# Performance work log

Hardware: AMD Instinct MI355X
Metric: run time of the kernel (lower is better)

Reference implementation:

```python
import jax, jax.numpy as jnp
import numpy as np

B, S, HID = 2, 2048, 2048
H, K, D = 32, 8, 64          # query heads, kv heads, head_dim
G = H // K                   # GQA group size
ROPE_MSCALE = 1.2            # constant rope_mscale applied to q and k
SM_SCALE = 1.0 / (D ** 0.5)  # flash_attn default softmax scale


def rotate_half(x):
    h = x.shape[-1] // 2
    return jnp.concatenate([-x[..., h:], x[..., :h]], axis=-1)


def setup_inputs() -> dict:
    key = jax.random.key(0)
    k1, k2, k3, k4 = jax.random.split(key, 4)
    hidden_states = jax.random.normal(k1, (B, S, HID), dtype=jnp.float32)
    # standard rotary tables: cos/sin of shape [S, D]
    inv_freq = 1.0 / (10000.0 ** (jnp.arange(0, D, 2, dtype=jnp.float32) / D))
    freqs = jnp.outer(jnp.arange(S, dtype=jnp.float32), inv_freq)  # [S, D/2]
    emb = jnp.concatenate([freqs, freqs], axis=-1)                 # [S, D]
    cos, sin = jnp.cos(emb), jnp.sin(emb)
    per_head_scale = 1.0 + 0.1 * jax.random.normal(k2, (B, H), dtype=jnp.float32)
    Wqkv = jax.random.normal(k3, ((H + 2 * K) * D, HID), dtype=jnp.float32) * (HID ** -0.5)
    Wo = jax.random.normal(k4, (HID, H * D), dtype=jnp.float32) * ((H * D) ** -0.5)
    return {"cos": cos, "sin": sin, "hidden_states": hidden_states,
            "per_head_scale": per_head_scale, "Wqkv": Wqkv, "Wo": Wo}


def reference(cos, sin, hidden_states, per_head_scale, Wqkv, Wo):
    # fused QKV projection (CastedLinear, no bias)
    qkv = jnp.einsum('bsh,oh->bso', hidden_states, Wqkv)          # [B,S,(H+2K)*D]
    qkv = qkv.reshape(B, S, H + 2 * K, D)
    q = qkv[:, :, :H]                 # [B,S,H,D]
    k = qkv[:, :, H:H + K]            # [B,S,K,D]
    v = qkv[:, :, H + K:]             # [B,S,K,D]
    # rotary embedding: cos/sin [S,D] -> broadcast over heads via [S,1,D]
    c = cos[:, None, :]
    s_ = sin[:, None, :]
    q = q * c + rotate_half(q) * s_
    k = k * c + rotate_half(k) * s_
    # rope_mscale
    q = q * ROPE_MSCALE
    k = k * ROPE_MSCALE
    # per-head scale on queries: [B,H] -> [B,1,H,1]
    q = q * per_head_scale[:, None, :, None]
    # GQA attention without materializing repeated K/V: group query heads
    qg = q.reshape(B, S, K, G, D)
    scores = jnp.einsum('bqkgd,bskd->bkgqs', qg, k) * SM_SCALE    # [B,K,G,Sq,Sk]
    causal = jnp.arange(S)[:, None] >= jnp.arange(S)[None, :]     # [Sq,Sk]
    scores = jnp.where(causal, scores, jnp.finfo(scores.dtype).min)
    probs = jax.nn.softmax(scores, axis=-1)
    out = jnp.einsum('bkgqs,bskd->bqkgd', probs, v).reshape(B, S, H * D)
    return jnp.einsum('bso,ho->bsh', out, Wo)                     # o_proj
```

## Files before the change

### kernel.cpp

```cpp
#include <hip/hip_runtime.h>
#include <stdint.h>

typedef unsigned short u16;
typedef short short8 __attribute__((ext_vector_type(8)));
typedef float f32x4 __attribute__((ext_vector_type(4)));
typedef uint32_t u32x4 __attribute__((ext_vector_type(4)));

#define S_LEN 2048
#define NQH 32
#define NKH 8
#define DHD 64
#define MNEG -1.0e30f

__device__ __forceinline__ float b2f(u16 u){
  union { uint32_t i; float f; } c; c.i = ((uint32_t)u) << 16; return c.f;
}
__device__ __forceinline__ u16 f2b(float f){
  union { float f; uint32_t i; } c; c.f = f;
  uint32_t r = c.i + 0x7fffu + ((c.i >> 16) & 1u);
  return (u16)(r >> 16);
}
__device__ __forceinline__ uint32_t cvt_pk_bf16(float lo, float hi){
  uint32_t r;
  asm("v_cvt_pk_bf16_f32 %0, %1, %2" : "=v"(r) : "v"(lo), "v"(hi));
  return r;
}
__device__ __forceinline__ void gload_lds16(const void* g, void* l){
  __builtin_amdgcn_global_load_lds((const __attribute__((address_space(1))) uint32_t*)g,
                                   (__attribute__((address_space(3))) uint32_t*)l, 16, 0, 0);
}

__global__ __launch_bounds__(256) void cvt_all(const float* __restrict__ hs,
                                               const float* __restrict__ wq,
                                               const float* __restrict__ wo,
                                               const float* __restrict__ cosp,
                                               const float* __restrict__ sinp,
                                               u16* __restrict__ hsB,
                                               u16* __restrict__ wqB,
                                               u16* __restrict__ woB,
                                               uint32_t* __restrict__ csB){
  int i = blockIdx.x * 256 + threadIdx.x;
  if (i >= 4718592){
    int off = i - 4718592;
    float4 c = ((const float4*)cosp)[off];
    float4 s = ((const float4*)sinp)[off];
    u32x4 o = { (uint32_t)f2b(c.x) | ((uint32_t)f2b(s.x) << 16),
                (uint32_t)f2b(c.y) | ((uint32_t)f2b(s.y) << 16),
                (uint32_t)f2b(c.z) | ((uint32_t)f2b(s.z) << 16),
                (uint32_t)f2b(c.w) | ((uint32_t)f2b(s.w) << 16) };
    ((u32x4*)csB)[off] = o;
    return;
  }
  const float* src; u16* dst; int off;
  if (i < 2097152)      { src = hs; dst = hsB; off = i; }
  else if (i < 3670016) { src = wq; dst = wqB; off = i - 2097152; }
  else                  { src = wo; dst = woB; off = i - 3670016; }
  float4 v = ((const float4*)src)[off];
  uint2 o;
  o.x = (uint32_t)f2b(v.x) | ((uint32_t)f2b(v.y) << 16);
  o.y = (uint32_t)f2b(v.z) | ((uint32_t)f2b(v.w) << 16);
  ((uint2*)dst)[off] = o;
}

template<int OUT_F32>
__global__ __launch_bounds__(256)
void gemm_bt(const u16* __restrict__ A, const u16* __restrict__ Bm,
             void* __restrict__ Cp, int N, int K)
{
  __shared__ alignas(16) u16 lA[128 * 64];
  __shared__ alignas(16) u16 lB[128 * 64];
  const int tid = threadIdx.x;
  const int w = tid >> 6, l = tid & 63;
  const int lg = l >> 4, lc = l & 15;
  const int wm = w >> 1, wn = w & 1;
  const int m0 = blockIdx.y * 128, n0 = blockIdx.x * 128;
  const int srow = l >> 3, sc = l & 7;
  const size_t ldb = (size_t)K * 2;
  f32x4 acc[4][4] = {};
  const int kiters = K >> 6;
  for (int kt = 0; kt < kiters; ++kt){
    __syncthreads();
#pragma unroll
    for (int i = 0; i < 4; ++i){
      const int row = (i * 4 + w) * 8 + srow;
      const int gc = ((sc ^ (row & 7)) << 4);
      gload_lds16((const char*)A + (size_t)(m0 + row) * ldb + (size_t)kt * 128 + gc,
                  (char*)lA + row * 128 + sc * 16);
    }
#pragma unroll
    for (int i = 0; i < 4; ++i){
      const int row = (i * 4 + w) * 8 + srow;
      const int gc = ((sc ^ (row & 7)) << 4);
      gload_lds16((const char*)Bm + (size_t)(n0 + row) * ldb + (size_t)kt * 128 + gc,
                  (char*)lB + row * 128 + sc * 16);
    }
    __syncthreads();
#pragma unroll
    for (int kk = 0; kk < 2; ++kk){
      short8 af[4], bfr[4];
#pragma unroll
      for (int mi = 0; mi < 4; ++mi){
        const int row = wm * 64 + mi * 16 + lc;
        const int cc = (kk * 4 + lg) ^ (row & 7);
        af[mi] = *(const short8*)((const char*)lA + row * 128 + cc * 16);
      }
#pragma unroll
      for (int ni = 0; ni < 4; ++ni){
        const int row = wn * 64 + ni * 16 + lc;
        const int cc = (kk * 4 + lg) ^ (row & 7);
        bfr[ni] = *(const short8*)((const char*)lB + row * 128 + cc * 16);
      }
#pragma unroll
      for (int mi = 0; mi < 4; ++mi)
#pragma unroll
        for (int ni = 0; ni < 4; ++ni)
          acc[mi][ni] = __builtin_amdgcn_mfma_f32_16x16x32_bf16(af[mi], bfr[ni], acc[mi][ni], 0, 0, 0);
    }
  }
  const int r0 = m0 + wm * 64 + lg * 4;
  const int c0 = n0 + wn * 64 + lc;
#pragma unroll
  for (int mi = 0; mi < 4; ++mi)
#pragma unroll
    for (int ni = 0; ni < 4; ++ni)
#pragma unroll
      for (int j = 0; j < 4; ++j){
        const size_t idx = (size_t)(r0 + mi * 16 + j) * (size_t)N + (size_t)(c0 + ni * 16);
        if (OUT_F32) ((float*)Cp)[idx] = acc[mi][ni][j];
        else         ((u16*)Cp)[idx]  = f2b(acc[mi][ni][j]);
      }
}

__global__ __launch_bounds__(256)
void gemm1_rope(const u16* __restrict__ A, const u16* __restrict__ Bm,
                const uint32_t* __restrict__ cs, const float* __restrict__ phs,
                u16* __restrict__ Qo, u16* __restrict__ Ko, u16* __restrict__ Vraw)
{
  __shared__ alignas(16) u16 lA[128 * 64];
  __shared__ alignas(16) u16 lB[128 * 64];
  const int tid = threadIdx.x;
  const int w = tid >> 6, l = tid & 63;
  const int lg = l >> 4, lc = l & 15;
  const int wm = w >> 1, wn = w & 1;
  const int m0 = blockIdx.y * 128, n0 = blockIdx.x * 128;
  const int srow = l >> 3, sc = l & 7;
  const size_t ldb = 4096;
  f32x4 acc[4][4] = {};
  for (int kt = 0; kt < 32; ++kt){
    __syncthreads();
#pragma unroll
    for (int i = 0; i < 4; ++i){
      const int row = (i * 4 + w) * 8 + srow;
      const int gc = ((sc ^ (row & 7)) << 4);
      gload_lds16((const char*)A + (size_t)(m0 + row) * ldb + (size_t)kt * 128 + gc,
                  (char*)lA + row * 128 + sc * 16);
    }
#pragma unroll
    for (int i = 0; i < 4; ++i){
      const int row = (i * 4 + w) * 8 + srow;
      const int gc = ((sc ^ (row & 7)) << 4);
      gload_lds16((const char*)Bm + (size_t)(n0 + row) * ldb + (size_t)kt * 128 + gc,
                  (char*)lB + row * 128 + sc * 16);
    }
    __syncthreads();
#pragma unroll
    for (int kk = 0; kk < 2; ++kk){
      short8 af[4], bfr[4];
#pragma unroll
      for (int mi = 0; mi < 4; ++mi){
        const int row = wm * 64 + mi * 16 + lc;
        const int cc = (kk * 4 + lg) ^ (row & 7);
        af[mi] = *(const short8*)((const char*)lA + row * 128 + cc * 16);
      }
#pragma unroll
      for (int ni = 0; ni < 4; ++ni){
        const int row = wn * 64 + ni * 16 + lc;
        const int cc = (kk * 4 + lg) ^ (row & 7);
        bfr[ni] = *(const short8*)((const char*)lB + row * 128 + cc * 16);
      }
#pragma unroll
      for (int mi = 0; mi < 4; ++mi)
#pragma unroll
        for (int ni = 0; ni < 4; ++ni)
          acc[mi][ni] = __builtin_amdgcn_mfma_f32_16x16x32_bf16(af[mi], bfr[ni], acc[mi][ni], 0, 0, 0);
    }
  }
  const int r0 = m0 + wm * 64 + lg * 4;
  const int c0 = n0 + wn * 64 + lc;
  const int head = (n0 + wn * 64) >> 6;
  const int b = m0 >> 11;
  if (head < 40){
    const float scale = (head < NQH) ? 1.2f * 0.18033688011112042f * phs[b * NQH + head] : 1.2f;
    u16* dstbase = (head < NQH)
        ? (Qo + ((size_t)(b * NQH + head) * S_LEN) * 64)
        : (Ko + ((size_t)(b * NKH + (head - NQH)) * S_LEN) * 64);
#pragma unroll
    for (int mi = 0; mi < 4; ++mi)
#pragma unroll
      for (int j = 0; j < 4; ++j){
        const int s = (r0 + mi * 16 + j) & 2047;
        const uint32_t* csrow = cs + s * 64;
        float xs[4] = {acc[mi][0][j], acc[mi][1][j], acc[mi][2][j], acc[mi][3][j]};
#pragma unroll
        for (int ni = 0; ni < 4; ++ni){
          const int d = lc + ni * 16;
          const uint32_t csv = csrow[d];
          const float cv = b2f((u16)(csv & 0xffff));
          const float sv = b2f((u16)(csv >> 16));
          const float sgn = (ni < 2) ? -1.f : 1.f;
          const float v = (xs[ni] * cv + sgn * xs[ni ^ 2] * sv) * scale;
          dstbase[(size_t)s * 64 + d] = f2b(v);
        }
      }
  } else {
#pragma unroll
    for (int mi = 0; mi < 4; ++mi)
#pragma unroll
      for (int ni = 0; ni < 4; ++ni)
#pragma unroll
        for (int j = 0; j < 4; ++j){
          const int r = r0 + mi * 16 + j;
          Vraw[(size_t)r * 512 + (c0 + ni * 16 - 2560)] = f2b(acc[mi][ni][j]);
        }
  }
}

__global__ __launch_bounds__(256)
void vtrans(const u16* __restrict__ Vraw, u16* __restrict__ VT)
{
  int bid = blockIdx.x;
  int t = bid & 15, kh = (bid >> 4) & 7, b = bid >> 7;
  __shared__ u16 vlds[128][72];
  int tid = threadIdx.x;
  {
    int r = tid >> 1, half = tid & 1;
    const u16* src = Vraw + (((size_t)(b * S_LEN + t * 128 + r) * 8 + kh) << 6) + half * 32;
    uint4 a0 = *(const uint4*)(src);
    uint4 a1 = *(const uint4*)(src + 8);
    uint4 a2 = *(const uint4*)(src + 16);
    uint4 a3 = *(const uint4*)(src + 24);
    *(uint4*)&vlds[r][half * 32]      = a0;
    *(uint4*)&vlds[r][half * 32 + 8]  = a1;
    *(uint4*)&vlds[r][half * 32 + 16] = a2;
    *(uint4*)&vlds[r][half * 32 + 24] = a3;
  }
  __syncthreads();
  const int d = tid >> 2, kk2 = tid & 3;
  u16* dst = VT + ((size_t)(b * NKH + kh) * 64 + d) * S_LEN + t * 128 + kk2 * 32;
#pragma unroll
  for (int j = 0; j < 4; ++j){
    u16 o[8];
#pragma unroll
    for (int e = 0; e < 8; ++e){
      const int hk = kk2 * 32 + ((e >> 2) << 4) + j * 4 + (e & 3);
      o[e] = vlds[hk][d];
    }
    uint4 ov = { (uint32_t)o[0] | ((uint32_t)o[1] << 16), (uint32_t)o[2] | ((uint32_t)o[3] << 16),
                 (uint32_t)o[4] | ((uint32_t)o[5] << 16), (uint32_t)o[6] | ((uint32_t)o[7] << 16) };
    *(uint4*)(dst + j * 8) = ov;
  }
}

__device__ __forceinline__ void proc_chunk(f32x4 (&sv)[8], float& mrow, float& lsum,
                                           f32x4 (&o)[4], uint32_t (&pw)[4][4],
                                           const int lg, const int lc,
                                           const bool diag, const int qloc)
{
  if (diag){
#pragma unroll
    for (int nj = 0; nj < 8; ++nj)
#pragma unroll
      for (int jj = 0; jj < 4; ++jj){
        const int kloc = nj * 16 + lg * 4 + jj;
        if (kloc > qloc) sv[nj][jj] = MNEG;
      }
  }
  float mu = sv[0][0];
#pragma unroll
  for (int nj = 0; nj < 8; ++nj)
#pragma unroll
    for (int jj = 0; jj < 4; ++jj) mu = fmaxf(mu, sv[nj][jj]);
  mu = fmaxf(mu, __shfl_xor(mu, 16));
  mu = fmaxf(mu, __shfl_xor(mu, 32));
  if (!__all(mu <= mrow + 11.54f)){
    const float mnew = fmaxf(mrow, mu);
    const float sf = __builtin_amdgcn_exp2f(mrow - mnew);
    mrow = mnew;
    lsum *= sf;
#pragma unroll
    for (int dn = 0; dn < 4; ++dn)
#pragma unroll
      for (int jj = 0; jj < 4; ++jj) o[dn][jj] *= sf;
  }
  const float mcur = mrow;
  float ps = 0.f;
#pragma unroll
  for (int nj = 0; nj < 8; ++nj)
#pragma unroll
    for (int jj = 0; jj < 4; ++jj){
      const float pv = __builtin_amdgcn_exp2f(sv[nj][jj] - mcur);
      sv[nj][jj] = pv;
      ps += pv;
    }
  lsum += ps;
#pragma unroll
  for (int kk2 = 0; kk2 < 4; ++kk2){
    pw[kk2][0] = cvt_pk_bf16(sv[kk2 * 2][0],     sv[kk2 * 2][1]);
    pw[kk2][1] = cvt_pk_bf16(sv[kk2 * 2][2],     sv[kk2 * 2][3]);
    pw[kk2][2] = cvt_pk_bf16(sv[kk2 * 2 + 1][0], sv[kk2 * 2 + 1][1]);
    pw[kk2][3] = cvt_pk_bf16(sv[kk2 * 2 + 1][2], sv[kk2 * 2 + 1][3]);
  }
}

__device__ __forceinline__ short8 pw_frag(const uint32_t* pw){
  u32x4 v = { pw[0], pw[1], pw[2], pw[3] };
  return __builtin_bit_cast(short8, v);
}

__global__ __launch_bounds__(512, 2)
void attn_kernel(const u16* __restrict__ Q, const u16* __restrict__ Kr,
                 const u16* __restrict__ VT, u16* __restrict__ Ao)
{
  int bid = blockIdx.x;
  int p  = bid & 15;
  int gp = (bid >> 4) & 1;
  int kh = (bid >> 5) & 7;
  int b  = bid >> 8;
  const int qt0 = p, qt1 = 31 - p;

  __shared__ alignas(16) u16 lK[2][128 * 64];
  __shared__ alignas(16) u16 lV[2][64 * 128];

  const int tid = threadIdx.x;
  const int hh = tid >> 8;
  const int h  = kh * 4 + gp * 2 + hh;
  const int w  = (tid >> 6) & 3;
  const int l  = tid & 63;
  const int lg = l >> 4, lc = l & 15;

  short8 qf[2][2];
  {
    const u16* qbase = Q + ((size_t)(b * NQH + h) * S_LEN) * 64;
#pragma unroll
    for (int kk = 0; kk < 2; ++kk){
      qf[0][kk] = *(const short8*)(qbase + (size_t)(qt0 * 64 + w * 16 + lc) * 64 + kk * 32 + lg * 8);
      qf[1][kk] = *(const short8*)(qbase + (size_t)(qt1 * 64 + w * 16 + lc) * 64 + kk * 32 + lg * 8);
    }
  }

  const u16* Kb = Kr + (size_t)(b * NKH + kh) * S_LEN * 64;
  const u16* Vb = VT + (size_t)(b * NKH + kh) * 64 * S_LEN;

  f32x4 o[2][4] = {};
  float mrow[2] = {MNEG, MNEG};
  float lsum[2] = {0.f, 0.f};

  const int nt = (qt1 >> 1) + 1;
  const int nt0 = qt0 >> 1;

#define STAGE(T, BSEL) do { \
    _Pragma("unroll") \
    for (int i_ = 0; i_ < 2; ++i_){ \
      const int row_ = i_ * 64 + (tid >> 3); \
      const int ch_  = tid & 7; \
      const int gc_  = ((ch_ ^ (row_ & 7)) << 4); \
      gload_lds16((const char*)(Kb + (size_t)((T) * 128 + row_) * 64) + gc_, \
                  (char*)lK[BSEL] + row_ * 128 + ch_ * 16); \
    } \
    _Pragma("unroll") \
    for (int i_ = 0; i_ < 2; ++i_){ \
      const int row_ = i_ * 32 + (tid >> 4); \
      const int ch_  = tid & 15; \
      const int gc_  = ((ch_ ^ (row_ & 15)) << 4); \
      gload_lds16((const char*)(Vb + (size_t)row_ * S_LEN + (T) * 128) + gc_, \
                  (char*)lV[BSEL] + row_ * 256 + ch_ * 16); \
    } \
  } while (0)

  STAGE(0, 0);

  for (int t = 0; t < nt; ++t){
    const int cur = t & 1;
    const bool act0 = (t <= nt0);
    if (t + 1 < nt){
      STAGE(t + 1, cur ^ 1);
      asm volatile("s_waitcnt vmcnt(4)" ::: "memory");
    } else {
      asm volatile("s_waitcnt vmcnt(0)" ::: "memory");
    }
    __builtin_amdgcn_s_barrier();

    f32x4 sv[2][8] = {};
    __builtin_amdgcn_s_setprio(1);
#pragma unroll
    for (int kk = 0; kk < 2; ++kk){
      short8 kf[8];
#pragma unroll
      for (int nj = 0; nj < 8; ++nj){
        const int row = nj * 16 + lc;
        const int cc = (kk * 4 + lg) ^ (row & 7);
        kf[nj] = *(const short8*)((const char*)lK[cur] + row * 128 + cc * 16);
      }
      if (act0)
#pragma unroll
        for (int nj = 0; nj < 8; ++nj)
          sv[0][nj] = __builtin_amdgcn_mfma_f32_16x16x32_bf16(kf[nj], qf[0][kk], sv[0][nj], 0, 0, 0);
#pragma unroll
      for (int nj = 0; nj < 8; ++nj)
        sv[1][nj] = __builtin_amdgcn_mfma_f32_16x16x32_bf16(kf[nj], qf[1][kk], sv[1][nj], 0, 0, 0);
    }
    __builtin_amdgcn_s_setprio(0);

    uint32_t pw[2][4][4];
    if (act0)
      proc_chunk(sv[0], mrow[0], lsum[0], o[0], pw[0], lg, lc,
                 t == (qt0 >> 1), (qt0 & 1) * 64 + w * 16 + lc);
    proc_chunk(sv[1], mrow[1], lsum[1], o[1], pw[1], lg, lc,
               t == (qt1 >> 1), (qt1 & 1) * 64 + w * 16 + lc);

    __builtin_amdgcn_s_setprio(1);
#pragma unroll
    for (int kk2 = 0; kk2 < 4; ++kk2){
      short8 vf[4];
#pragma unroll
      for (int dn = 0; dn < 4; ++dn){
        const int row = dn * 16 + lc;
        const int cc = (kk2 * 4 + lg) ^ (row & 15);
        vf[dn] = *(const short8*)((const char*)lV[cur] + row * 256 + cc * 16);
      }
      if (act0){
        const short8 pb0 = pw_frag(pw[0][kk2]);
#pragma unroll
        for (int dn = 0; dn < 4; ++dn)
          o[0][dn] = __builtin_amdgcn_mfma_f32_16x16x32_bf16(vf[dn], pb0, o[0][dn], 0, 0, 0);
      }
      const short8 pb1 = pw_frag(pw[1][kk2]);
#pragma unroll
      for (int dn = 0; dn < 4; ++dn)
        o[1][dn] = __builtin_amdgcn_mfma_f32_16x16x32_bf16(vf[dn], pb1, o[1][dn], 0, 0, 0);
    }
    __builtin_amdgcn_s_setprio(0);
    __builtin_amdgcn_s_barrier();
  }
#undef STAGE

#pragma unroll
  for (int c = 0; c < 2; ++c){
    const int qt = c ? qt1 : qt0;
    float ls = lsum[c];
    ls += __shfl_xor(ls, 16);
    ls += __shfl_xor(ls, 32);
    const float inv = 1.f / ls;
    const int sq = qt * 64 + w * 16 + lc;
#pragma unroll
    for (int dn = 0; dn < 4; ++dn){
      uint2 pk;
      pk.x = cvt_pk_bf16(o[c][dn][0] * inv, o[c][dn][1] * inv);
      pk.y = cvt_pk_bf16(o[c][dn][2] * inv, o[c][dn][3] * inv);
      const int col = h * 64 + dn * 16 + lg * 4;
      *(uint2*)&Ao[(size_t)(b * S_LEN + sq) * 2048 + col] = pk;
    }
  }
}

extern "C" void kernel_launch(void* const* d_in, const int* in_sizes, int n_in,
                              void* d_out, int out_size, void* d_ws, size_t ws_size,
                              hipStream_t stream)
{
  const float* cosT = (const float*)d_in[0];
  const float* sinT = (const float*)d_in[1];
  const float* hs   = (const float*)d_in[2];
  const float* phs  = (const float*)d_in[3];
  const float* Wqkv = (const float*)d_in[4];
  const float* Wo   = (const float*)d_in[5];
  float* out = (float*)d_out;
  char* ws = (char*)d_ws;

  u16* hsB   = (u16*)(ws);
  u16* WqkvB = (u16*)(ws + 16777216);
  u16* WoB   = (u16*)(ws + 29360128);
  u16* Vraw  = (u16*)(ws + 37748736);
  u16* Qb    = (u16*)(ws + 41943040);
  u16* Kb    = (u16*)(ws + 58720256);
  u16* VTb   = (u16*)(ws + 62914560);
  uint32_t* csB = (uint32_t*)(ws + 67108864);
  u16* Ao    = hsB;

  cvt_all<<<18560, 256, 0, stream>>>(hs, Wqkv, Wo, cosT, sinT, hsB, WqkvB, WoB, csB);
  gemm1_rope<<<dim3(24, 32), 256, 0, stream>>>(hsB, WqkvB, csB, phs, Qb, Kb, Vraw);
  vtrans<<<256, 256, 0, stream>>>(Vraw, VTb);
  attn_kernel<<<512, 512, 0, stream>>>(Qb, Kb, VTb, Ao);
  gemm_bt<1><<<dim3(16, 32), 256, 0, stream>>>(Ao, WoB, (void*)out, 2048, 2048);
}
```

Before: 224.8 us.

## Double-buffer LDS in projection GEMMs and remap blocks for XCD locality

Both the QKV+RoPE GEMM and the output-projection GEMM now use two LDS buffers. The next K-tile's global-to-LDS loads are issued before the current tile's MFMAs, with a partial vmcnt wait, so memory latency overlaps compute. Launches also change to a 1D grid with a swizzled block-to-tile mapping that places neighbouring tiles on the same XCD to improve L2 reuse. LDS per block doubles to 64KB, which may reduce occupancy.

```diff
diff --git a/kernel.cpp b/kernel.cpp
--- a/kernel.cpp
+++ b/kernel.cpp
@@ -62,39 +62,51 @@
   ((uint2*)dst)[off] = o;
 }
 
-template<int OUT_F32>
+#define GSTAGE(KT, BSEL) do { \
+    _Pragma("unroll") \
+    for (int i_ = 0; i_ < 4; ++i_){ \
+      const int row_ = (i_ * 4 + w) * 8 + srow; \
+      const int gc_ = ((sc ^ (row_ & 7)) << 4); \
+      gload_lds16((const char*)A + (size_t)(m0 + row_) * ldb + (size_t)(KT) * 128 + gc_, \
+                  (char*)lA + (BSEL) * 16384 + row_ * 128 + sc * 16); \
+    } \
+    _Pragma("unroll") \
+    for (int i_ = 0; i_ < 4; ++i_){ \
+      const int row_ = (i_ * 4 + w) * 8 + srow; \
+      const int gc_ = ((sc ^ (row_ & 7)) << 4); \
+      gload_lds16((const char*)Bm + (size_t)(n0 + row_) * ldb + (size_t)(KT) * 128 + gc_, \
+                  (char*)lB + (BSEL) * 16384 + row_ * 128 + sc * 16); \
+    } \
+  } while (0)
+
 __global__ __launch_bounds__(256)
-void gemm_bt(const u16* __restrict__ A, const u16* __restrict__ Bm,
-             void* __restrict__ Cp, int N, int K)
+void gemm_bt_f32(const u16* __restrict__ A, const u16* __restrict__ Bm,
+                 float* __restrict__ Cp, int N, int K, int nbx, int nwg)
 {
-  __shared__ alignas(16) u16 lA[128 * 64];
-  __shared__ alignas(16) u16 lB[128 * 64];
+  __shared__ alignas(16) u16 lA[2 * 128 * 64];
+  __shared__ alignas(16) u16 lB[2 * 128 * 64];
+  const int id = blockIdx.x;
+  const int swz = (id & 7) * (nwg >> 3) + (id >> 3);
+  const int m0 = (swz / nbx) * 128, n0 = (swz % nbx) * 128;
   const int tid = threadIdx.x;
   const int w = tid >> 6, l = tid & 63;
   const int lg = l >> 4, lc = l & 15;
   const int wm = w >> 1, wn = w & 1;
-  const int m0 = blockIdx.y * 128, n0 = blockIdx.x * 128;
   const int srow = l >> 3, sc = l & 7;
   const size_t ldb = (size_t)K * 2;
   f32x4 acc[4][4] = {};
   const int kiters = K >> 6;
+
+  GSTAGE(0, 0);
   for (int kt = 0; kt < kiters; ++kt){
-    __syncthreads();
-#pragma unroll
-    for (int i = 0; i < 4; ++i){
-      const int row = (i * 4 + w) * 8 + srow;
-      const int gc = ((sc ^ (row & 7)) << 4);
-      gload_lds16((const char*)A + (size_t)(m0 + row) * ldb + (size_t)kt * 128 + gc,
-                  (char*)lA + row * 128 + sc * 16);
-    }
-#pragma unroll
-    for (int i = 0; i < 4; ++i){
-      const int row = (i * 4 + w) * 8 + srow;
-      const int gc = ((sc ^ (row & 7)) << 4);
-      gload_lds16((const char*)Bm + (size_t)(n0 + row) * ldb + (size_t)kt * 128 + gc,
-                  (char*)lB + row * 128 + sc * 16);
-    }
-    __syncthreads();
+    const int cur = kt & 1;
+    if (kt + 1 < kiters){
+      GSTAGE(kt + 1, cur ^ 1);
+      asm volatile("s_waitcnt vmcnt(8)" ::: "memory");
+    } else {
+      asm volatile("s_waitcnt vmcnt(0)" ::: "memory");
+    }
+    __builtin_amdgcn_s_barrier();
 #pragma unroll
     for (int kk = 0; kk < 2; ++kk){
       short8 af[4], bfr[4];
@@ -102,13 +114,13 @@
       for (int mi = 0; mi < 4; ++mi){
         const int row = wm * 64 + mi * 16 + lc;
         const int cc = (kk * 4 + lg) ^ (row & 7);
-        af[mi] = *(const short8*)((const char*)lA + row * 128 + cc * 16);
+        af[mi] = *(const short8*)((const char*)lA + cur * 16384 + row * 128 + cc * 16);
       }
 #pragma unroll
       for (int ni = 0; ni < 4; ++ni){
         const int row = wn * 64 + ni * 16 + lc;
         const int cc = (kk * 4 + lg) ^ (row & 7);
-        bfr[ni] = *(const short8*)((const char*)lB + row * 128 + cc * 16);
+        bfr[ni] = *(const short8*)((const char*)lB + cur * 16384 + row * 128 + cc * 16);
       }
 #pragma unroll
       for (int mi = 0; mi < 4; ++mi)
@@ -116,6 +128,7 @@
         for (int ni = 0; ni < 4; ++ni)
           acc[mi][ni] = __builtin_amdgcn_mfma_f32_16x16x32_bf16(af[mi], bfr[ni], acc[mi][ni], 0, 0, 0);
     }
+    __builtin_amdgcn_s_barrier();
   }
   const int r0 = m0 + wm * 64 + lg * 4;
   const int c0 = n0 + wn * 64 + lc;
@@ -124,11 +137,8 @@
 #pragma unroll
     for (int ni = 0; ni < 4; ++ni)
 #pragma unroll
-      for (int j = 0; j < 4; ++j){
-        const size_t idx = (size_t)(r0 + mi * 16 + j) * (size_t)N + (size_t)(c0 + ni * 16);
-        if (OUT_F32) ((float*)Cp)[idx] = acc[mi][ni][j];
-        else         ((u16*)Cp)[idx]  = f2b(acc[mi][ni][j]);
-      }
+      for (int j = 0; j < 4; ++j)
+        Cp[(size_t)(r0 + mi * 16 + j) * (size_t)N + (size_t)(c0 + ni * 16)] = acc[mi][ni][j];
 }
 
 __global__ __launch_bounds__(256)
@@ -136,33 +146,29 @@
                 const uint32_t* __restrict__ cs, const float* __restrict__ phs,
                 u16* __restrict__ Qo, u16* __restrict__ Ko, u16* __restrict__ Vraw)
 {
-  __shared__ alignas(16) u16 lA[128 * 64];
-  __shared__ alignas(16) u16 lB[128 * 64];
+  __shared__ alignas(16) u16 lA[2 * 128 * 64];
+  __shared__ alignas(16) u16 lB[2 * 128 * 64];
+  const int id = blockIdx.x;
+  const int swz = (id & 7) * 96 + (id >> 3);
+  const int m0 = (swz / 24) * 128, n0 = (swz % 24) * 128;
   const int tid = threadIdx.x;
   const int w = tid >> 6, l = tid & 63;
   const int lg = l >> 4, lc = l & 15;
   const int wm = w >> 1, wn = w & 1;
-  const int m0 = blockIdx.y * 128, n0 = blockIdx.x * 128;
   const int srow = l >> 3, sc = l & 7;
   const size_t ldb = 4096;
   f32x4 acc[4][4] = {};
+
+  GSTAGE(0, 0);
   for (int kt = 0; kt < 32; ++kt){
-    __syncthreads();
-#pragma unroll
-    for (int i = 0; i < 4; ++i){
-      const int row = (i * 4 + w) * 8 + srow;
-      const int gc = ((sc ^ (row & 7)) << 4);
-      gload_lds16((const char*)A + (size_t)(m0 + row) * ldb + (size_t)kt * 128 + gc,
-                  (char*)lA + row * 128 + sc * 16);
-    }
-#pragma unroll
-    for (int i = 0; i < 4; ++i){
-      const int row = (i * 4 + w) * 8 + srow;
-      const int gc = ((sc ^ (row & 7)) << 4);
-      gload_lds16((const char*)Bm + (size_t)(n0 + row) * ldb + (size_t)kt * 128 + gc,
-                  (char*)lB + row * 128 + sc * 16);
-    }
-    __syncthreads();
+    const int cur = kt & 1;
+    if (kt + 1 < 32){
+      GSTAGE(kt + 1, cur ^ 1);
+      asm volatile("s_waitcnt vmcnt(8)" ::: "memory");
+    } else {
+      asm volatile("s_waitcnt vmcnt(0)" ::: "memory");
+    }
+    __builtin_amdgcn_s_barrier();
 #pragma unroll
     for (int kk = 0; kk < 2; ++kk){
       short8 af[4], bfr[4];
@@ -170,13 +176,13 @@
       for (int mi = 0; mi < 4; ++mi){
         const int row = wm * 64 + mi * 16 + lc;
         const int cc = (kk * 4 + lg) ^ (row & 7);
-        af[mi] = *(const short8*)((const char*)lA + row * 128 + cc * 16);
+        af[mi] = *(const short8*)((const char*)lA + cur * 16384 + row * 128 + cc * 16);
       }
 #pragma unroll
       for (int ni = 0; ni < 4; ++ni){
         const int row = wn * 64 + ni * 16 + lc;
         const int cc = (kk * 4 + lg) ^ (row & 7);
-        bfr[ni] = *(const short8*)((const char*)lB + row * 128 + cc * 16);
+        bfr[ni] = *(const short8*)((const char*)lB + cur * 16384 + row * 128 + cc * 16);
       }
 #pragma unroll
       for (int mi = 0; mi < 4; ++mi)
@@ -184,6 +190,7 @@
         for (int ni = 0; ni < 4; ++ni)
           acc[mi][ni] = __builtin_amdgcn_mfma_f32_16x16x32_bf16(af[mi], bfr[ni], acc[mi][ni], 0, 0, 0);
     }
+    __builtin_amdgcn_s_barrier();
   }
   const int r0 = m0 + wm * 64 + lg * 4;
   const int c0 = n0 + wn * 64 + lc;
@@ -224,6 +231,7 @@
         }
   }
 }
+#undef GSTAGE
 
 __global__ __launch_bounds__(256)
 void vtrans(const u16* __restrict__ Vraw, u16* __restrict__ VT)
@@ -487,8 +495,8 @@
   u16* Ao    = hsB;
 
   cvt_all<<<18560, 256, 0, stream>>>(hs, Wqkv, Wo, cosT, sinT, hsB, WqkvB, WoB, csB);
-  gemm1_rope<<<dim3(24, 32), 256, 0, stream>>>(hsB, WqkvB, csB, phs, Qb, Kb, Vraw);
+  gemm1_rope<<<768, 256, 0, stream>>>(hsB, WqkvB, csB, phs, Qb, Kb, Vraw);
   vtrans<<<256, 256, 0, stream>>>(Vraw, VTb);
   attn_kernel<<<512, 512, 0, stream>>>(Qb, Kb, VTb, Ao);
-  gemm_bt<1><<<dim3(16, 32), 256, 0, stream>>>(Ao, WoB, (void*)out, 2048, 2048);
-}
+  gemm_bt_f32<<<512, 256, 0, stream>>>(Ao, WoB, out, 2048, 2048, 16, 512);
+}
```

Measured after the change: 215.4 us. 1.04x faster.
